# Kernel optimization log

Hardware: AMD Instinct MI355X
Metric: run time of the kernel (lower is better)

Reference implementation:

```python
import jax, jax.numpy as jnp
import numpy as np

F_, E_, B_, D_, H_, O_ = 4, 8, 4096, 512, 1024, 512


def setup_inputs() -> dict:
    key = jax.random.key(0)
    ks = jax.random.split(key, 7)
    s = 0.02  # small init scale to keep activations sane
    return {
        "features": jax.random.normal(ks[0], (F_, B_, D_), jnp.float32),
        "W1": jax.random.normal(ks[1], (F_, E_, D_, H_), jnp.float32) * s,
        "b1": jax.random.normal(ks[2], (F_, E_, H_), jnp.float32) * s,
        "W2": jax.random.normal(ks[3], (F_, E_, H_, O_), jnp.float32) * s,
        "b2": jax.random.normal(ks[4], (F_, E_, O_), jnp.float32) * s,
        "Wg": jax.random.normal(ks[5], (F_, D_, E_), jnp.float32) * s,
        "bg": jax.random.normal(ks[6], (F_, E_), jnp.float32) * s,
    }


def reference(features, W1, b1, W2, b2, Wg, bg):
    # Gate: softmax over experts, per feature. [F,B,E]
    gate = jax.nn.softmax(jnp.einsum('fbd,fde->fbe', features, Wg) + bg[:, None, :], axis=-1)
    # All experts computed densely (soft MoE): hidden [F,B,E,H]
    h = jax.nn.relu(jnp.einsum('fbd,fedh->fbeh', features, W1) + b1[:, None, :, :])
    # Expert outputs [F,B,E,O]
    eo = jnp.einsum('fbeh,feho->fbeo', h, W2) + b2[:, None, :, :]
    # Gate-weighted sum over experts, then mean over features -> [B,O]
    weighted = jnp.einsum('fbe,fbeo->fbo', gate, eo)
    return jnp.mean(weighted, axis=0)
```

## Files before the change

kernel.cpp:

```cpp
#include <hip/hip_runtime.h>


#define F_ 4
#define E_ 8
#define B_ 4096
#define D_ 512
#define H_ 1024
#define O_ 512

typedef unsigned short ushort_t;
typedef __bf16 bf16x8 __attribute__((ext_vector_type(8)));
typedef float f32x4 __attribute__((ext_vector_type(4)));
typedef unsigned short ushort8_t __attribute__((ext_vector_type(8)));

__device__ inline ushort_t f2bf(float f) {
  union { float f; unsigned u; } v; v.f = f;
  unsigned r = v.u + 0x7FFFu + ((v.u >> 16) & 1u);
  return (ushort_t)(r >> 16);
}
__device__ inline float bf2f(ushort_t u) {
  union { unsigned u; float f; } v; v.u = ((unsigned)u) << 16;
  return v.f;
}

__device__ inline void async16(const void* g, void* l) {
  __builtin_amdgcn_global_load_lds(
      (const __attribute__((address_space(1))) unsigned int*)g,
      (__attribute__((address_space(3))) unsigned int*)l, 16, 0, 0);
}

__global__ void cast_feat_kernel(const float* __restrict__ in, ushort_t* __restrict__ out) {
  const int i = blockIdx.x * 256 + threadIdx.x;
  const float4 v = ((const float4*)in)[i];
  ushort4 o;
  o.x = f2bf(v.x); o.y = f2bf(v.y); o.z = f2bf(v.z); o.w = f2bf(v.w);
  ((ushort4*)out)[i] = o;
}

__global__ void transpose_cast_kernel(const float* __restrict__ in, ushort_t* __restrict__ out,
                                      int R, int C) {
  __shared__ float tile[64][65];
  const size_t zoff = (size_t)blockIdx.z * R * C;
  in += zoff; out += zoff;
  const int tx = threadIdx.x & 63, ty = threadIdx.x >> 6;
  const int r0 = blockIdx.y * 64, c0 = blockIdx.x * 64;
#pragma unroll
  for (int i = 0; i < 16; ++i) {
    const int r = ty + i * 4;
    tile[r][tx] = in[(size_t)(r0 + r) * C + c0 + tx];
  }
  __syncthreads();
#pragma unroll
  for (int i = 0; i < 16; ++i) {
    const int c = ty + i * 4;
    out[(size_t)(c0 + c) * R + r0 + tx] = f2bf(tile[tx][c]);
  }
}

__global__ void gate_kernel(const float* __restrict__ features, const float* __restrict__ Wg,
                            const float* __restrict__ bg, float* __restrict__ g2) {
  const int fb = blockIdx.x;
  const int f = fb >> 12, b = fb & (B_ - 1);
  const int lane = threadIdx.x;
  const float* feat = features + ((size_t)f * B_ + b) * D_;
  const float* wg = Wg + (size_t)f * D_ * E_;
  float acc[E_] = {0.f, 0.f, 0.f, 0.f, 0.f, 0.f, 0.f, 0.f};
  for (int d = lane; d < D_; d += 64) {
    const float fv = feat[d];
    const float4 w0 = ((const float4*)(wg + d * E_))[0];
    const float4 w1 = ((const float4*)(wg + d * E_))[1];
    acc[0] += fv * w0.x; acc[1] += fv * w0.y; acc[2] += fv * w0.z; acc[3] += fv * w0.w;
    acc[4] += fv * w1.x; acc[5] += fv * w1.y; acc[6] += fv * w1.z; acc[7] += fv * w1.w;
  }
#pragma unroll
  for (int off = 32; off >= 1; off >>= 1)
#pragma unroll
    for (int e = 0; e < E_; ++e) acc[e] += __shfl_xor(acc[e], off, 64);
  float lg[E_], mx = -1e30f;
#pragma unroll
  for (int e = 0; e < E_; ++e) { lg[e] = acc[e] + bg[f * E_ + e]; mx = fmaxf(mx, lg[e]); }
  float s = 0.f;
#pragma unroll
  for (int e = 0; e < E_; ++e) { lg[e] = __expf(lg[e] - mx); s += lg[e]; }
  const float inv = 1.f / (s * (float)F_);
  if (lane < E_) g2[((size_t)f * B_ + b) * E_ + lane] = lg[lane] * inv;
}

__global__ __launch_bounds__(256, 4) void gemm1_kernel(
    const ushort_t* __restrict__ A, const ushort_t* __restrict__ Bt,
    const float* __restrict__ b1, const float* __restrict__ g2,
    ushort_t* __restrict__ Hf) {
  __shared__ ushort_t As[128 * 32];
  __shared__ ushort_t Bs[128 * 32];
  const int id = blockIdx.x;
  const int e = id & 7;
  const int s = id >> 3;
  const int n0 = (s & 7) * 128;
  const int m0 = (s >> 3) * 128;
  const ushort_t* Bp = Bt + (size_t)e * H_ * D_;

  const int t = threadIdx.x, lane = t & 63, w = t >> 6;
  const int wm = w & 1, wn = w >> 1;
  const int lr = lane & 15, q = lane >> 4;
  const int pc = q ^ ((lr >> 1) & 3);

  const int r0 = t >> 2;
  const int g = (t & 3) ^ ((r0 >> 1) & 3);
  const char* aSrc0 = (const char*)A + (size_t)(m0 + r0) * (D_ * 2) + g * 16;
  const char* aSrc1 = (const char*)A + (size_t)(m0 + r0 + 64) * (D_ * 2) + g * 16;
  const char* bSrc0 = (const char*)Bp + (size_t)(n0 + r0) * (D_ * 2) + g * 16;
  const char* bSrc1 = (const char*)Bp + (size_t)(n0 + r0 + 64) * (D_ * 2) + g * 16;
  ushort_t* aDst0 = &As[t * 8];  ushort_t* aDst1 = &As[2048 + t * 8];
  ushort_t* bDst0 = &Bs[t * 8];  ushort_t* bDst1 = &Bs[2048 + t * 8];

  f32x4 acc[4][4];
#pragma unroll
  for (int i = 0; i < 4; ++i)
#pragma unroll
    for (int j = 0; j < 4; ++j) acc[i][j] = (f32x4){0.f, 0.f, 0.f, 0.f};

  for (int ks = 0; ks < D_ / 32; ++ks) {
    async16(aSrc0, aDst0); async16(aSrc1, aDst1);
    async16(bSrc0, bDst0); async16(bSrc1, bDst1);
    aSrc0 += 64; aSrc1 += 64; bSrc0 += 64; bSrc1 += 64;
    __syncthreads();
    bf16x8 af[4], bfr[4];
#pragma unroll
    for (int i = 0; i < 4; ++i)
      af[i] = *(const bf16x8*)&As[(wm * 64 + i * 16 + lr) * 32 + pc * 8];
#pragma unroll
    for (int j = 0; j < 4; ++j)
      bfr[j] = *(const bf16x8*)&Bs[(wn * 64 + j * 16 + lr) * 32 + pc * 8];
#pragma unroll
    for (int i = 0; i < 4; ++i)
#pragma unroll
      for (int j = 0; j < 4; ++j)
        acc[i][j] = __builtin_amdgcn_mfma_f32_16x16x32_bf16(bfr[j], af[i], acc[i][j], 0, 0, 0);
    __syncthreads();
  }

  const float* b1e = b1 + (size_t)e * H_;
#pragma unroll
  for (int i = 0; i < 4; ++i) {
    const int m = m0 + wm * 64 + i * 16 + lr;
    const float gv = g2[m * E_ + e];
    ushort_t* dstRow = Hf + ((size_t)e * B_ + m) * H_ + n0 + wn * 64 + q * 4;
#pragma unroll
    for (int j = 0; j < 4; ++j) {
      const int n = n0 + wn * 64 + j * 16 + q * 4;
      const float4 bb = *(const float4*)&b1e[n];
      ushort4 o;
      o.x = f2bf(fmaxf(acc[i][j][0] + bb.x, 0.f) * gv);
      o.y = f2bf(fmaxf(acc[i][j][1] + bb.y, 0.f) * gv);
      o.z = f2bf(fmaxf(acc[i][j][2] + bb.z, 0.f) * gv);
      o.w = f2bf(fmaxf(acc[i][j][3] + bb.w, 0.f) * gv);
      *(ushort4*)(dstRow + j * 16) = o;
    }
  }
}

__global__ __launch_bounds__(256, 4) void gemm2_kernel(
    const ushort_t* __restrict__ Hf, const ushort_t* __restrict__ Bt,
    const float* __restrict__ b2, const float* __restrict__ g2,
    ushort_t* __restrict__ part) {
  __shared__ ushort_t As[128 * 32];
  __shared__ ushort_t Bs[128 * 32];
  const int id = blockIdx.x;
  const int grp = id & 3;
  const int s = id >> 2;
  const int n0 = (s & 3) * 128;
  const int m0 = (s >> 2) * 128;
  const int e0 = grp * 2;

  const int t = threadIdx.x, lane = t & 63, w = t >> 6;
  const int wm = w & 1, wn = w >> 1;
  const int lr = lane & 15, q = lane >> 4;
  const int pc = q ^ ((lr >> 1) & 3);

  const int r0 = t >> 2;
  const int g = (t & 3) ^ ((r0 >> 1) & 3);
  ushort_t* aDst0 = &As[t * 8];  ushort_t* aDst1 = &As[2048 + t * 8];
  ushort_t* bDst0 = &Bs[t * 8];  ushort_t* bDst1 = &Bs[2048 + t * 8];

  f32x4 acc[4][4];
#pragma unroll
  for (int i = 0; i < 4; ++i)
#pragma unroll
    for (int j = 0; j < 4; ++j) acc[i][j] = (f32x4){0.f, 0.f, 0.f, 0.f};

  for (int h = 0; h < 2; ++h) {
    const int e = e0 + h;
    const ushort_t* Ap = Hf + (size_t)e * B_ * H_;
    const ushort_t* Bp = Bt + (size_t)e * O_ * H_;
    const char* aSrc0 = (const char*)Ap + (size_t)(m0 + r0) * (H_ * 2) + g * 16;
    const char* aSrc1 = (const char*)Ap + (size_t)(m0 + r0 + 64) * (H_ * 2) + g * 16;
    const char* bSrc0 = (const char*)Bp + (size_t)(n0 + r0) * (H_ * 2) + g * 16;
    const char* bSrc1 = (const char*)Bp + (size_t)(n0 + r0 + 64) * (H_ * 2) + g * 16;
    for (int ks = 0; ks < H_ / 32; ++ks) {
      async16(aSrc0, aDst0); async16(aSrc1, aDst1);
      async16(bSrc0, bDst0); async16(bSrc1, bDst1);
      aSrc0 += 64; aSrc1 += 64; bSrc0 += 64; bSrc1 += 64;
      __syncthreads();
      bf16x8 af[4], bfr[4];
#pragma unroll
      for (int i = 0; i < 4; ++i)
        af[i] = *(const bf16x8*)&As[(wm * 64 + i * 16 + lr) * 32 + pc * 8];
#pragma unroll
      for (int j = 0; j < 4; ++j)
        bfr[j] = *(const bf16x8*)&Bs[(wn * 64 + j * 16 + lr) * 32 + pc * 8];
#pragma unroll
      for (int i = 0; i < 4; ++i)
#pragma unroll
        for (int j = 0; j < 4; ++j)
          acc[i][j] = __builtin_amdgcn_mfma_f32_16x16x32_bf16(bfr[j], af[i], acc[i][j], 0, 0, 0);
      __syncthreads();
    }
  }

  const float* b2e0 = b2 + (size_t)e0 * O_;
  const float* b2e1 = b2e0 + O_;
#pragma unroll
  for (int i = 0; i < 4; ++i) {
    const int m = m0 + wm * 64 + i * 16 + lr;
    const float gv0 = g2[m * E_ + e0];
    const float gv1 = g2[m * E_ + e0 + 1];
    ushort_t* dstRow = part + (size_t)grp * (B_ * O_) + (size_t)m * O_ + n0 + wn * 64 + q * 4;
#pragma unroll
    for (int j = 0; j < 4; ++j) {
      const int n = n0 + wn * 64 + j * 16 + q * 4;
      const float4 c0 = *(const float4*)&b2e0[n];
      const float4 c1 = *(const float4*)&b2e1[n];
      ushort4 o;
      o.x = f2bf(acc[i][j][0] + gv0 * c0.x + gv1 * c1.x);
      o.y = f2bf(acc[i][j][1] + gv0 * c0.y + gv1 * c1.y);
      o.z = f2bf(acc[i][j][2] + gv0 * c0.z + gv1 * c1.z);
      o.w = f2bf(acc[i][j][3] + gv0 * c0.w + gv1 * c1.w);
      *(ushort4*)(dstRow + j * 16) = o;
    }
  }
}

__global__ void reduce_kernel(const ushort_t* __restrict__ part, float* __restrict__ out) {
  const size_t p = ((size_t)blockIdx.x * 256 + threadIdx.x) * 8;
  float s[8] = {0.f, 0.f, 0.f, 0.f, 0.f, 0.f, 0.f, 0.f};
#pragma unroll
  for (int k = 0; k < F_ * 4; ++k) {
    const ushort8_t u = *(const ushort8_t*)&part[(size_t)k * (B_ * O_) + p];
#pragma unroll
    for (int j = 0; j < 8; ++j) s[j] += bf2f(u[j]);
  }
  float4 o0 = {s[0], s[1], s[2], s[3]}, o1 = {s[4], s[5], s[6], s[7]};
  *(float4*)&out[p] = o0;
  *(float4*)&out[p + 4] = o1;
}

extern "C" void kernel_launch(void* const* d_in, const int* in_sizes, int n_in,
                              void* d_out, int out_size, void* d_ws, size_t ws_size,
                              hipStream_t stream) {
  const float* features = (const float*)d_in[0];
  const float* W1 = (const float*)d_in[1];
  const float* b1 = (const float*)d_in[2];
  const float* W2 = (const float*)d_in[3];
  const float* b2 = (const float*)d_in[4];
  const float* Wg = (const float*)d_in[5];
  const float* bg = (const float*)d_in[6];
  float* out = (float*)d_out;

  char* ws = (char*)d_ws;
  ushort_t* featbf = (ushort_t*)ws;
  ushort_t* w1t    = (ushort_t*)(ws + 16777216);
  ushort_t* w2t    = (ushort_t*)(ws + 50331648);
  float*    g2     = (float*)(ws + 83886080);
  ushort_t* Hf     = (ushort_t*)(ws + 84410368);
  ushort_t* part   = (ushort_t*)(ws + 151519232);

  cast_feat_kernel<<<F_ * B_ * D_ / 1024, 256, 0, stream>>>(features, featbf);
  transpose_cast_kernel<<<dim3(H_ / 64, D_ / 64, F_ * E_), 256, 0, stream>>>(W1, w1t, D_, H_);
  transpose_cast_kernel<<<dim3(O_ / 64, H_ / 64, F_ * E_), 256, 0, stream>>>(W2, w2t, H_, O_);
  gate_kernel<<<F_ * B_, 64, 0, stream>>>(features, Wg, bg, g2);

  for (int f = 0; f < F_; ++f) {
    gemm1_kernel<<<(B_ / 128) * (H_ / 128) * E_, 256, 0, stream>>>(
        featbf + (size_t)f * B_ * D_,
        w1t + (size_t)f * E_ * H_ * D_,
        b1 + (size_t)f * E_ * H_,
        g2 + (size_t)f * B_ * E_,
        Hf);
    gemm2_kernel<<<(B_ / 128) * (O_ / 128) * 4, 256, 0, stream>>>(
        Hf,
        w2t + (size_t)f * E_ * O_ * H_,
        b2 + (size_t)f * E_ * O_,
        g2 + (size_t)f * B_ * E_,
        part + (size_t)f * 4 * B_ * O_);
  }
  reduce_kernel<<<B_ * O_ / 8 / 256, 256, 0, stream>>>(part, out);
}
```

Baseline: 653.0 us.

## Widen GEMM K-tile to 64, stage epilogue through LDS, batch features in grid

```diff
diff --git a/kernel.cpp b/kernel.cpp
--- a/kernel.cpp
+++ b/kernel.cpp
@@ -29,12 +29,44 @@
       (__attribute__((address_space(3))) unsigned int*)l, 16, 0, 0);
 }
 
-__global__ void cast_feat_kernel(const float* __restrict__ in, ushort_t* __restrict__ out) {
-  const int i = blockIdx.x * 256 + threadIdx.x;
-  const float4 v = ((const float4*)in)[i];
-  ushort4 o;
-  o.x = f2bf(v.x); o.y = f2bf(v.y); o.z = f2bf(v.z); o.w = f2bf(v.w);
-  ((ushort4*)out)[i] = o;
+__global__ void prep_kernel(const float* __restrict__ features, const float* __restrict__ Wg,
+                            const float* __restrict__ bg, float* __restrict__ g2,
+                            ushort_t* __restrict__ featbf) {
+  const int fb = blockIdx.x;
+  const int f = fb >> 12, b = fb & (B_ - 1);
+  const int lane = threadIdx.x;
+  const float* feat = features + ((size_t)f * B_ + b) * D_;
+  const float* wg = Wg + (size_t)f * D_ * E_;
+  const int d0 = lane * 8;
+  float ff[8];
+  *(float4*)&ff[0] = *(const float4*)&feat[d0];
+  *(float4*)&ff[4] = *(const float4*)&feat[d0 + 4];
+  ushort8_t u;
+#pragma unroll
+  for (int k = 0; k < 8; ++k) u[k] = f2bf(ff[k]);
+  *(ushort8_t*)&featbf[((size_t)f * B_ + b) * D_ + d0] = u;
+
+  float acc[E_] = {0.f, 0.f, 0.f, 0.f, 0.f, 0.f, 0.f, 0.f};
+#pragma unroll
+  for (int k = 0; k < 8; ++k) {
+    const float fv = ff[k];
+    const float4 w0 = ((const float4*)(wg + (size_t)(d0 + k) * E_))[0];
+    const float4 w1 = ((const float4*)(wg + (size_t)(d0 + k) * E_))[1];
+    acc[0] += fv * w0.x; acc[1] += fv * w0.y; acc[2] += fv * w0.z; acc[3] += fv * w0.w;
+    acc[4] += fv * w1.x; acc[5] += fv * w1.y; acc[6] += fv * w1.z; acc[7] += fv * w1.w;
+  }
+#pragma unroll
+  for (int off = 32; off >= 1; off >>= 1)
+#pragma unroll
+    for (int e = 0; e < E_; ++e) acc[e] += __shfl_xor(acc[e], off, 64);
+  float lg[E_], mx = -1e30f;
+#pragma unroll
+  for (int e = 0; e < E_; ++e) { lg[e] = acc[e] + bg[f * E_ + e]; mx = fmaxf(mx, lg[e]); }
+  float s = 0.f;
+#pragma unroll
+  for (int e = 0; e < E_; ++e) { lg[e] = __expf(lg[e] - mx); s += lg[e]; }
+  const float inv = 1.f / (s * (float)F_);
+  if (lane < E_) g2[((size_t)f * B_ + b) * E_ + lane] = lg[lane] * inv;
 }
 
 __global__ void transpose_cast_kernel(const float* __restrict__ in, ushort_t* __restrict__ out,
@@ -57,61 +89,34 @@
   }
 }
 
-__global__ void gate_kernel(const float* __restrict__ features, const float* __restrict__ Wg,
-                            const float* __restrict__ bg, float* __restrict__ g2) {
-  const int fb = blockIdx.x;
-  const int f = fb >> 12, b = fb & (B_ - 1);
-  const int lane = threadIdx.x;
-  const float* feat = features + ((size_t)f * B_ + b) * D_;
-  const float* wg = Wg + (size_t)f * D_ * E_;
-  float acc[E_] = {0.f, 0.f, 0.f, 0.f, 0.f, 0.f, 0.f, 0.f};
-  for (int d = lane; d < D_; d += 64) {
-    const float fv = feat[d];
-    const float4 w0 = ((const float4*)(wg + d * E_))[0];
-    const float4 w1 = ((const float4*)(wg + d * E_))[1];
-    acc[0] += fv * w0.x; acc[1] += fv * w0.y; acc[2] += fv * w0.z; acc[3] += fv * w0.w;
-    acc[4] += fv * w1.x; acc[5] += fv * w1.y; acc[6] += fv * w1.z; acc[7] += fv * w1.w;
-  }
-#pragma unroll
-  for (int off = 32; off >= 1; off >>= 1)
-#pragma unroll
-    for (int e = 0; e < E_; ++e) acc[e] += __shfl_xor(acc[e], off, 64);
-  float lg[E_], mx = -1e30f;
-#pragma unroll
-  for (int e = 0; e < E_; ++e) { lg[e] = acc[e] + bg[f * E_ + e]; mx = fmaxf(mx, lg[e]); }
-  float s = 0.f;
-#pragma unroll
-  for (int e = 0; e < E_; ++e) { lg[e] = __expf(lg[e] - mx); s += lg[e]; }
-  const float inv = 1.f / (s * (float)F_);
-  if (lane < E_) g2[((size_t)f * B_ + b) * E_ + lane] = lg[lane] * inv;
-}
-
-__global__ __launch_bounds__(256, 4) void gemm1_kernel(
-    const ushort_t* __restrict__ A, const ushort_t* __restrict__ Bt,
+
+__global__ __launch_bounds__(256, 3) void gemm1_kernel(
+    const ushort_t* __restrict__ featbf, const ushort_t* __restrict__ w1t,
     const float* __restrict__ b1, const float* __restrict__ g2,
-    ushort_t* __restrict__ Hf) {
-  __shared__ ushort_t As[128 * 32];
-  __shared__ ushort_t Bs[128 * 32];
+    ushort_t* __restrict__ Hf, int f0, size_t hfStride) {
+  __shared__ __align__(16) ushort_t buf[128 * 136];
+  ushort_t* As = buf;
+  ushort_t* Bs = buf + 8192;
+  const int fy = blockIdx.y, f = f0 + fy;
   const int id = blockIdx.x;
   const int e = id & 7;
   const int s = id >> 3;
   const int n0 = (s & 7) * 128;
   const int m0 = (s >> 3) * 128;
-  const ushort_t* Bp = Bt + (size_t)e * H_ * D_;
+  const ushort_t* A  = featbf + (size_t)f * B_ * D_;
+  const ushort_t* Bp = w1t + ((size_t)f * E_ + e) * H_ * D_;
+  const float* b1e = b1 + ((size_t)f * E_ + e) * H_;
+  const float* g2f = g2 + (size_t)f * B_ * E_;
+  ushort_t* HfF = Hf + (size_t)fy * hfStride + (size_t)e * B_ * H_;
 
   const int t = threadIdx.x, lane = t & 63, w = t >> 6;
   const int wm = w & 1, wn = w >> 1;
   const int lr = lane & 15, q = lane >> 4;
-  const int pc = q ^ ((lr >> 1) & 3);
-
-  const int r0 = t >> 2;
-  const int g = (t & 3) ^ ((r0 >> 1) & 3);
-  const char* aSrc0 = (const char*)A + (size_t)(m0 + r0) * (D_ * 2) + g * 16;
-  const char* aSrc1 = (const char*)A + (size_t)(m0 + r0 + 64) * (D_ * 2) + g * 16;
-  const char* bSrc0 = (const char*)Bp + (size_t)(n0 + r0) * (D_ * 2) + g * 16;
-  const char* bSrc1 = (const char*)Bp + (size_t)(n0 + r0 + 64) * (D_ * 2) + g * 16;
-  ushort_t* aDst0 = &As[t * 8];  ushort_t* aDst1 = &As[2048 + t * 8];
-  ushort_t* bDst0 = &Bs[t * 8];  ushort_t* bDst1 = &Bs[2048 + t * 8];
+
+  const int rr = t >> 3;
+  const int lc = (t & 7) ^ (rr & 7);
+  const char* aSrc = (const char*)A + (size_t)(m0 + rr) * (D_ * 2) + lc * 16;
+  const char* bSrc = (const char*)Bp + (size_t)(n0 + rr) * (D_ * 2) + lc * 16;
 
   f32x4 acc[4][4];
 #pragma unroll
@@ -119,68 +124,80 @@
 #pragma unroll
     for (int j = 0; j < 4; ++j) acc[i][j] = (f32x4){0.f, 0.f, 0.f, 0.f};
 
-  for (int ks = 0; ks < D_ / 32; ++ks) {
-    async16(aSrc0, aDst0); async16(aSrc1, aDst1);
-    async16(bSrc0, bDst0); async16(bSrc1, bDst1);
-    aSrc0 += 64; aSrc1 += 64; bSrc0 += 64; bSrc1 += 64;
+  for (int ks = 0; ks < D_ / 64; ++ks) {
+#pragma unroll
+    for (int p = 0; p < 4; ++p) {
+      async16(aSrc + (size_t)p * (32 * D_ * 2), &As[t * 8 + p * 2048]);
+      async16(bSrc + (size_t)p * (32 * D_ * 2), &Bs[t * 8 + p * 2048]);
+    }
+    aSrc += 128; bSrc += 128;
     __syncthreads();
-    bf16x8 af[4], bfr[4];
-#pragma unroll
-    for (int i = 0; i < 4; ++i)
-      af[i] = *(const bf16x8*)&As[(wm * 64 + i * 16 + lr) * 32 + pc * 8];
-#pragma unroll
-    for (int j = 0; j < 4; ++j)
-      bfr[j] = *(const bf16x8*)&Bs[(wn * 64 + j * 16 + lr) * 32 + pc * 8];
-#pragma unroll
-    for (int i = 0; i < 4; ++i)
+#pragma unroll
+    for (int kh = 0; kh < 2; ++kh) {
+      const int ca = (((kh << 2) | q) ^ (lr & 7)) * 8;
+      bf16x8 af[4], bfr[4];
+#pragma unroll
+      for (int i = 0; i < 4; ++i)
+        af[i] = *(const bf16x8*)&As[(wm * 64 + i * 16 + lr) * 64 + ca];
 #pragma unroll
       for (int j = 0; j < 4; ++j)
-        acc[i][j] = __builtin_amdgcn_mfma_f32_16x16x32_bf16(bfr[j], af[i], acc[i][j], 0, 0, 0);
+        bfr[j] = *(const bf16x8*)&Bs[(wn * 64 + j * 16 + lr) * 64 + ca];
+#pragma unroll
+      for (int i = 0; i < 4; ++i)
+#pragma unroll
+        for (int j = 0; j < 4; ++j)
+          acc[i][j] = __builtin_amdgcn_mfma_f32_16x16x32_bf16(bfr[j], af[i], acc[i][j], 0, 0, 0);
+    }
     __syncthreads();
   }
 
-  const float* b1e = b1 + (size_t)e * H_;
 #pragma unroll
   for (int i = 0; i < 4; ++i) {
-    const int m = m0 + wm * 64 + i * 16 + lr;
-    const float gv = g2[m * E_ + e];
-    ushort_t* dstRow = Hf + ((size_t)e * B_ + m) * H_ + n0 + wn * 64 + q * 4;
+    const int ml = wm * 64 + i * 16 + lr;
+    const float gv = g2f[(m0 + ml) * E_ + e];
 #pragma unroll
     for (int j = 0; j < 4; ++j) {
-      const int n = n0 + wn * 64 + j * 16 + q * 4;
-      const float4 bb = *(const float4*)&b1e[n];
+      const int nl = wn * 64 + j * 16 + q * 4;
+      const float4 bb = *(const float4*)&b1e[n0 + nl];
       ushort4 o;
       o.x = f2bf(fmaxf(acc[i][j][0] + bb.x, 0.f) * gv);
       o.y = f2bf(fmaxf(acc[i][j][1] + bb.y, 0.f) * gv);
       o.z = f2bf(fmaxf(acc[i][j][2] + bb.z, 0.f) * gv);
       o.w = f2bf(fmaxf(acc[i][j][3] + bb.w, 0.f) * gv);
-      *(ushort4*)(dstRow + j * 16) = o;
-    }
-  }
-}
-
-__global__ __launch_bounds__(256, 4) void gemm2_kernel(
-    const ushort_t* __restrict__ Hf, const ushort_t* __restrict__ Bt,
+      *(ushort4*)&buf[ml * 136 + nl] = o;
+    }
+  }
+  __syncthreads();
+  const int row = t >> 1, half = t & 1;
+  const ushort_t* src = &buf[row * 136 + half * 64];
+  ushort_t* dst = HfF + (size_t)(m0 + row) * H_ + n0 + half * 64;
+#pragma unroll
+  for (int c = 0; c < 8; ++c)
+    *(ushort8_t*)(dst + c * 8) = *(const ushort8_t*)(src + c * 8);
+}
+
+__global__ __launch_bounds__(256, 3) void gemm2_kernel(
+    const ushort_t* __restrict__ Hf, const ushort_t* __restrict__ w2t,
     const float* __restrict__ b2, const float* __restrict__ g2,
-    ushort_t* __restrict__ part) {
-  __shared__ ushort_t As[128 * 32];
-  __shared__ ushort_t Bs[128 * 32];
+    ushort_t* __restrict__ part, int f0, size_t hfStride) {
+  __shared__ __align__(16) ushort_t buf[128 * 136];
+  ushort_t* As = buf;
+  ushort_t* Bs = buf + 8192;
+  const int fy = blockIdx.y, f = f0 + fy;
   const int id = blockIdx.x;
   const int grp = id & 3;
   const int s = id >> 2;
   const int n0 = (s & 3) * 128;
   const int m0 = (s >> 2) * 128;
   const int e0 = grp * 2;
+  const float* g2f = g2 + (size_t)f * B_ * E_;
 
   const int t = threadIdx.x, lane = t & 63, w = t >> 6;
   const int wm = w & 1, wn = w >> 1;
   const int lr = lane & 15, q = lane >> 4;
-  const int pc = q ^ ((lr >> 1) & 3);
-
-  const int r0 = t >> 2;
-  const int g = (t & 3) ^ ((r0 >> 1) & 3);
-  ushort_t* aDst0 = &As[t * 8];  ushort_t* aDst1 = &As[2048 + t * 8];
-  ushort_t* bDst0 = &Bs[t * 8];  ushort_t* bDst1 = &Bs[2048 + t * 8];
+
+  const int rr = t >> 3;
+  const int lc = (t & 7) ^ (rr & 7);
 
   f32x4 acc[4][4];
 #pragma unroll
@@ -190,44 +207,49 @@
 
   for (int h = 0; h < 2; ++h) {
     const int e = e0 + h;
-    const ushort_t* Ap = Hf + (size_t)e * B_ * H_;
-    const ushort_t* Bp = Bt + (size_t)e * O_ * H_;
-    const char* aSrc0 = (const char*)Ap + (size_t)(m0 + r0) * (H_ * 2) + g * 16;
-    const char* aSrc1 = (const char*)Ap + (size_t)(m0 + r0 + 64) * (H_ * 2) + g * 16;
-    const char* bSrc0 = (const char*)Bp + (size_t)(n0 + r0) * (H_ * 2) + g * 16;
-    const char* bSrc1 = (const char*)Bp + (size_t)(n0 + r0 + 64) * (H_ * 2) + g * 16;
-    for (int ks = 0; ks < H_ / 32; ++ks) {
-      async16(aSrc0, aDst0); async16(aSrc1, aDst1);
-      async16(bSrc0, bDst0); async16(bSrc1, bDst1);
-      aSrc0 += 64; aSrc1 += 64; bSrc0 += 64; bSrc1 += 64;
+    const char* aSrc = (const char*)(Hf + (size_t)fy * hfStride + (size_t)e * B_ * H_) +
+                       (size_t)(m0 + rr) * (H_ * 2) + lc * 16;
+    const char* bSrc = (const char*)(w2t + ((size_t)f * E_ + e) * O_ * H_) +
+                       (size_t)(n0 + rr) * (H_ * 2) + lc * 16;
+    for (int ks = 0; ks < H_ / 64; ++ks) {
+#pragma unroll
+      for (int p = 0; p < 4; ++p) {
+        async16(aSrc + (size_t)p * (32 * H_ * 2), &As[t * 8 + p * 2048]);
+        async16(bSrc + (size_t)p * (32 * H_ * 2), &Bs[t * 8 + p * 2048]);
+      }
+      aSrc += 128; bSrc += 128;
       __syncthreads();
-      bf16x8 af[4], bfr[4];
-#pragma unroll
-      for (int i = 0; i < 4; ++i)
-        af[i] = *(const bf16x8*)&As[(wm * 64 + i * 16 + lr) * 32 + pc * 8];
-#pragma unroll
-      for (int j = 0; j < 4; ++j)
-        bfr[j] = *(const bf16x8*)&Bs[(wn * 64 + j * 16 + lr) * 32 + pc * 8];
-#pragma unroll
-      for (int i = 0; i < 4; ++i)
+#pragma unroll
+      for (int kh = 0; kh < 2; ++kh) {
+        const int ca = (((kh << 2) | q) ^ (lr & 7)) * 8;
+        bf16x8 af[4], bfr[4];
+#pragma unroll
+        for (int i = 0; i < 4; ++i)
+          af[i] = *(const bf16x8*)&As[(wm * 64 + i * 16 + lr) * 64 + ca];
 #pragma unroll
         for (int j = 0; j < 4; ++j)
-          acc[i][j] = __builtin_amdgcn_mfma_f32_16x16x32_bf16(bfr[j], af[i], acc[i][j], 0, 0, 0);
+          bfr[j] = *(const bf16x8*)&Bs[(wn * 64 + j * 16 + lr) * 64 + ca];
+#pragma unroll
+        for (int i = 0; i < 4; ++i)
+#pragma unroll
+          for (int j = 0; j < 4; ++j)
+            acc[i][j] = __builtin_amdgcn_mfma_f32_16x16x32_bf16(bfr[j], af[i], acc[i][j], 0, 0, 0);
+      }
       __syncthreads();
     }
   }
 
-  const float* b2e0 = b2 + (size_t)e0 * O_;
+  const float* b2e0 = b2 + ((size_t)f * E_ + e0) * O_;
   const float* b2e1 = b2e0 + O_;
 #pragma unroll
   for (int i = 0; i < 4; ++i) {
-    const int m = m0 + wm * 64 + i * 16 + lr;
-    const float gv0 = g2[m * E_ + e0];
-    const float gv1 = g2[m * E_ + e0 + 1];
-    ushort_t* dstRow = part + (size_t)grp * (B_ * O_) + (size_t)m * O_ + n0 + wn * 64 + q * 4;
+    const int ml = wm * 64 + i * 16 + lr;
+    const float gv0 = g2f[(m0 + ml) * E_ + e0];
+    const float gv1 = g2f[(m0 + ml) * E_ + e0 + 1];
 #pragma unroll
     for (int j = 0; j < 4; ++j) {
-      const int n = n0 + wn * 64 + j * 16 + q * 4;
+      const int nl = wn * 64 + j * 16 + q * 4;
+      const int n = n0 + nl;
       const float4 c0 = *(const float4*)&b2e0[n];
       const float4 c1 = *(const float4*)&b2e1[n];
       ushort4 o;
@@ -235,9 +257,16 @@
       o.y = f2bf(acc[i][j][1] + gv0 * c0.y + gv1 * c1.y);
       o.z = f2bf(acc[i][j][2] + gv0 * c0.z + gv1 * c1.z);
       o.w = f2bf(acc[i][j][3] + gv0 * c0.w + gv1 * c1.w);
-      *(ushort4*)(dstRow + j * 16) = o;
-    }
-  }
+      *(ushort4*)&buf[ml * 136 + nl] = o;
+    }
+  }
+  __syncthreads();
+  const int row = t >> 1, half = t & 1;
+  const ushort_t* src = &buf[row * 136 + half * 64];
+  ushort_t* dst = part + (size_t)(f * 4 + grp) * (B_ * O_) + (size_t)(m0 + row) * O_ + n0 + half * 64;
+#pragma unroll
+  for (int c = 0; c < 8; ++c)
+    *(ushort8_t*)(dst + c * 8) = *(const ushort8_t*)(src + c * 8);
 }
 
 __global__ void reduce_kernel(const ushort_t* __restrict__ part, float* __restrict__ out) {
@@ -272,26 +301,26 @@
   ushort_t* w2t    = (ushort_t*)(ws + 50331648);
   float*    g2     = (float*)(ws + 83886080);
   ushort_t* Hf     = (ushort_t*)(ws + 84410368);
-  ushort_t* part   = (ushort_t*)(ws + 151519232);
-
-  cast_feat_kernel<<<F_ * B_ * D_ / 1024, 256, 0, stream>>>(features, featbf);
+  const bool big = ws_size >= (size_t)419954688;
+  ushort_t* part   = big ? (ushort_t*)(ws + 352845824)
+                         : (ushort_t*)(ws + 151519232);
+
+  prep_kernel<<<F_ * B_, 64, 0, stream>>>(features, Wg, bg, g2, featbf);
   transpose_cast_kernel<<<dim3(H_ / 64, D_ / 64, F_ * E_), 256, 0, stream>>>(W1, w1t, D_, H_);
   transpose_cast_kernel<<<dim3(O_ / 64, H_ / 64, F_ * E_), 256, 0, stream>>>(W2, w2t, H_, O_);
-  gate_kernel<<<F_ * B_, 64, 0, stream>>>(features, Wg, bg, g2);
-
-  for (int f = 0; f < F_; ++f) {
-    gemm1_kernel<<<(B_ / 128) * (H_ / 128) * E_, 256, 0, stream>>>(
-        featbf + (size_t)f * B_ * D_,
-        w1t + (size_t)f * E_ * H_ * D_,
-        b1 + (size_t)f * E_ * H_,
-        g2 + (size_t)f * B_ * E_,
-        Hf);
-    gemm2_kernel<<<(B_ / 128) * (O_ / 128) * 4, 256, 0, stream>>>(
-        Hf,
-        w2t + (size_t)f * E_ * O_ * H_,
-        b2 + (size_t)f * E_ * O_,
-        g2 + (size_t)f * B_ * E_,
-        part + (size_t)f * 4 * B_ * O_);
+
+  if (big) {
+    gemm1_kernel<<<dim3((B_ / 128) * (H_ / 128) * E_, F_), 256, 0, stream>>>(
+        featbf, w1t, b1, g2, Hf, 0, (size_t)E_ * B_ * H_);
+    gemm2_kernel<<<dim3((B_ / 128) * (O_ / 128) * 4, F_), 256, 0, stream>>>(
+        Hf, w2t, b2, g2, part, 0, (size_t)E_ * B_ * H_);
+  } else {
+    for (int f = 0; f < F_; ++f) {
+      gemm1_kernel<<<dim3((B_ / 128) * (H_ / 128) * E_, 1), 256, 0, stream>>>(
+          featbf, w1t, b1, g2, Hf, f, 0);
+      gemm2_kernel<<<dim3((B_ / 128) * (O_ / 128) * 4, 1), 256, 0, stream>>>(
+          Hf, w2t, b2, g2, part, f, 0);
+    }
   }
   reduce_kernel<<<B_ * O_ / 8 / 256, 256, 0, stream>>>(part, out);
 }
```

Measured after the change: 640.5 us. No clear change (-1.9%).
